# Optimization experiments

Measured on AMD Instinct MI355X. Metric: run time of the kernel, lower is better.

## Reference

```python
import jax, jax.numpy as jnp
import numpy as np

N, D, K = 16384, 256, 4096  # encoded vectors, embedding_dim, codebook_size


def setup_inputs() -> dict:
    key = jax.random.key(0)
    k_ze, k_cb = jax.random.split(key)
    ze = jax.random.normal(k_ze, (N, D), dtype=jnp.float32)
    codebook = jax.random.normal(k_cb, (K, D), dtype=jnp.float32)
    return {"ze": ze, "codebook": codebook}


def reference(ze, codebook):
    # Pairwise squared distances: ||ze||^2 + ||e||^2 - 2 ze e^T  -> [N, K]
    sq_norm = (
        jnp.sum(ze ** 2, axis=-1, keepdims=True)
        + jnp.sum(codebook ** 2, axis=1)
        - 2.0 * jnp.matmul(ze, codebook.T)
    )
    indices = jnp.argmin(sq_norm, axis=-1)            # [N]
    zq = jnp.take(codebook, indices, axis=0)          # [N, D] gather

    # VQ losses (stop-gradient mirrors .detach())
    vq_e_loss = jnp.mean((zq - jax.lax.stop_gradient(ze)) ** 2)
    vq_commit_loss = jnp.mean((jax.lax.stop_gradient(zq) - ze) ** 2)

    # perplexity: probs[i] = count_i / 10 (faithful to original, incl. /10)
    counts = jnp.zeros((K,), dtype=jnp.float32).at[indices].add(1.0)
    probs = counts / 10.0
    perplexity = jnp.exp(-jnp.sum(probs * jnp.log(probs + 1e-10)))

    return indices, zq, vq_e_loss, vq_commit_loss, perplexity
```

## Files before the change

### kernel.cpp

```cpp
#include <hip/hip_runtime.h>
#include <math.h>

#define N_TOT 16384
#define DIM   256
#define KCB   4096

typedef __attribute__((ext_vector_type(8)))  short s8v;
typedef __attribute__((ext_vector_type(16))) float f16v;

#define PK_OFF   32832
#define CBF_OFF  163904
#define WS_NEED  4358208ull
#define ZERO_W   36880

__device__ __forceinline__ void gload16(const void* g, void* l) {
  __builtin_amdgcn_global_load_lds(
      (const __attribute__((address_space(1))) unsigned int*)g,
      (__attribute__((address_space(3))) unsigned int*)l, 16, 0, 0);
}

__global__ __launch_bounds__(256)
void cb_prep_k(const float* __restrict__ cb, float* __restrict__ ws) {
  const int t = threadIdx.x, tile = blockIdx.x;
  for (int i = tile * 256 + t; i < ZERO_W; i += 128 * 256) ws[KCB + i] = 0.0f;

  const int col = t >> 3, j = t & 7;
  const int c0  = tile * 32;
  ushort* tb = (ushort*)((char*)ws + CBF_OFF) + (size_t)tile * 16384;
  const float* src = cb + (size_t)(c0 + col) * DIM;
  float s = 0.0f;
  #pragma unroll
  for (int ks = 0; ks < 16; ++ks) {
    #pragma unroll
    for (int kh = 0; kh < 2; ++kh) {
      float x = src[ks * 16 + kh * 8 + j];
      s += x * x;
      unsigned xb = __float_as_uint(x);
      unsigned hb = xb & 0xFFFF0000u;
      float lf = x - __uint_as_float(hb);
      tb[ks * 512 + kh * 256 + t]        = (ushort)(xb >> 16);
      tb[8192 + ks * 512 + kh * 256 + t] = (ushort)(__float_as_uint(lf) >> 16);
    }
  }
  s += __shfl_down(s, 4, 8);
  s += __shfl_down(s, 2, 8);
  s += __shfl_down(s, 1, 8);
  if (j == 0) ws[c0 + col] = s;
}

#define AP 260

__global__ __launch_bounds__(256, 2)
void vq_mfma_k(const float* __restrict__ ze, float* __restrict__ ws) {
  __shared__ __align__(16) char ldsU[65536];

  const int t    = threadIdx.x;
  const int lane = t & 63;
  const int w    = t >> 6;
  const int ln31 = lane & 31;
  const int hl   = lane >> 5;
  const int mb   = blockIdx.x >> 2;
  const int cq   = blockIdx.x & 3;
  const int m0   = mb * 128;

  const float* cbn = ws;
  unsigned long long* pk = (unsigned long long*)((char*)ws + PK_OFF);
  const char* cbF = (const char*)ws + CBF_OFF;

  s8v ah[16], al[16];
  float* Af = (float*)ldsU;
  for (int c = 0; c < 4; ++c) {
    __syncthreads();
    {
      int r  = t >> 3;
      int f0 = t & 7;
      const float* src = ze + (size_t)(m0 + c * 32 + r) * DIM;
      #pragma unroll
      for (int i = 0; i < 8; ++i) {
        int f = f0 + 8 * i;
        *(float4*)&Af[r * AP + f * 4] = *(const float4*)(src + f * 4);
      }
    }
    __syncthreads();
    if (w == c) {
      int rl = ln31;
      #pragma unroll
      for (int ks = 0; ks < 16; ++ks) {
        float4 x0 = *(const float4*)&Af[rl * AP + ks * 16 + hl * 8];
        float4 x1 = *(const float4*)&Af[rl * AP + ks * 16 + hl * 8 + 4];
        float xs[8] = {x0.x, x0.y, x0.z, x0.w, x1.x, x1.y, x1.z, x1.w};
        #pragma unroll
        for (int j = 0; j < 8; ++j) {
          unsigned xb = __float_as_uint(xs[j]);
          unsigned hb = xb & 0xFFFF0000u;
          float lf = xs[j] - __uint_as_float(hb);
          ah[ks][j] = (short)(xb >> 16);
          al[ks][j] = (short)(__float_as_uint(lf) >> 16);
        }
      }
    }
  }
  __syncthreads();

  char* bufs0 = ldsU;
  char* bufs1 = ldsU + 32768;
  const char* qbase = cbF + (size_t)cq * 32 * 32768;

  {
    const char* g = qbase + (size_t)w * 8192 + (size_t)lane * 16;
    char* lp = bufs0 + w * 8192;
    #pragma unroll
    for (int ii = 0; ii < 8; ++ii) gload16(g + ii * 1024, lp + ii * 1024);
  }

  float best[16];
  int   bidx[16];
  #pragma unroll
  for (int r = 0; r < 16; ++r) { best[r] = -1e30f; bidx[r] = 0; }

  #pragma unroll 1
  for (int tt = 0; tt < 32; ++tt) {
    __syncthreads();
    if (tt + 1 < 32) {
      const char* g = qbase + (size_t)(tt + 1) * 32768 + (size_t)w * 8192 + (size_t)lane * 16;
      char* lp = ((tt + 1) & 1 ? bufs1 : bufs0) + w * 8192;
      #pragma unroll
      for (int ii = 0; ii < 8; ++ii) gload16(g + ii * 1024, lp + ii * 1024);
    }

    const int   c0      = cq * 1024 + tt * 32;
    const float half_cv = 0.5f * cbn[c0 + ln31];
    const char* bc      = (tt & 1) ? bufs1 : bufs0;

    f16v hh, xx;
    #pragma unroll
    for (int r = 0; r < 16; ++r) { hh[r] = 0.0f; xx[r] = 0.0f; }

    #pragma unroll
    for (int ks = 0; ks < 16; ++ks) {
      s8v bh = *(const s8v*)(bc + ks * 1024 + lane * 16);
      s8v bl = *(const s8v*)(bc + 16384 + ks * 1024 + lane * 16);
      hh = __builtin_amdgcn_mfma_f32_32x32x16_bf16(ah[ks], bh, hh, 0, 0, 0);
      xx = __builtin_amdgcn_mfma_f32_32x32x16_bf16(ah[ks], bl, xx, 0, 0, 0);
      xx = __builtin_amdgcn_mfma_f32_32x32x16_bf16(al[ks], bh, xx, 0, 0, 0);
    }

    #pragma unroll
    for (int r = 0; r < 16; ++r) {
      float s = hh[r] + xx[r] - half_cv;
      if (s > best[r]) { best[r] = s; bidx[r] = c0 + ln31; }
    }
  }

  #pragma unroll
  for (int r = 0; r < 16; ++r) {
    float s = best[r];
    int   c = bidx[r];
    #pragma unroll
    for (int mk = 1; mk < 32; mk <<= 1) {
      float os = __shfl_xor(s, mk, 64);
      int   oc = __shfl_xor(c, mk, 64);
      if (os > s || (os == s && oc < c)) { s = os; c = oc; }
    }
    if (ln31 == 0) {
      int row = m0 + w * 32 + (r & 3) + 8 * (r >> 2) + 4 * hl;
      unsigned u = __float_as_uint(s);
      unsigned enc = (u & 0x80000000u) ? ~u : (u | 0x80000000u);
      unsigned long long p = ((unsigned long long)enc << 32) | (unsigned)(KCB - 1 - c);
      atomicMax(&pk[row], p);
    }
  }
}

__global__ __launch_bounds__(256)
void gather_k(const float* __restrict__ ze, const float* __restrict__ cb,
              float* __restrict__ ws, float* __restrict__ out) {
  __shared__ int sIdx[64];
  const int t  = threadIdx.x;
  const int m0 = blockIdx.x * 64;
  float* counts   = ws + KCB;
  float* loss_sum = ws + 2 * KCB;
  const unsigned long long* pk = (const unsigned long long*)((const char*)ws + PK_OFF);

  if (t < 64) {
    unsigned long long p = pk[m0 + t];
    int col = KCB - 1 - (int)(unsigned)(p & 0xFFFFFFFFull);
    out[m0 + t] = (float)col;
    sIdx[t] = col;
    atomicAdd(&counts[col], 1.0f);
  }
  __syncthreads();

  float* out_zq = out + N_TOT;
  const int w = t >> 6, ln = t & 63;
  float lsum = 0.0f;
  #pragma unroll
  for (int p = 0; p < 16; ++p) {
    int r = w + 4 * p;
    float4 cvv = *(const float4*)(cb + (size_t)sIdx[r] * DIM + ln * 4);
    float4 zv  = *(const float4*)(ze + (size_t)(m0 + r) * DIM + ln * 4);
    *(float4*)(out_zq + (size_t)(m0 + r) * DIM + ln * 4) = cvv;
    float dx = cvv.x - zv.x, dy = cvv.y - zv.y, dz = cvv.z - zv.z, dw = cvv.w - zv.w;
    lsum += dx * dx + dy * dy + dz * dz + dw * dw;
  }
  #pragma unroll
  for (int off = 32; off > 0; off >>= 1) lsum += __shfl_down(lsum, off, 64);
  if (ln == 0) atomicAdd(loss_sum, lsum);
}

__global__ void zero_ws_k(float* __restrict__ ws, int nw) {
  int i = blockIdx.x * 256 + threadIdx.x;
  if (i < nw) ws[KCB + i] = 0.0f;
}

__global__ void cbnorm_k(const float* __restrict__ cb, float* __restrict__ ws) {
  int row  = blockIdx.x * 4 + (threadIdx.x >> 6);
  int lane = threadIdx.x & 63;
  float4 v = *(const float4*)(cb + (size_t)row * DIM + lane * 4);
  float s = v.x*v.x + v.y*v.y + v.z*v.z + v.w*v.w;
  #pragma unroll
  for (int off = 32; off > 0; off >>= 1) s += __shfl_down(s, off, 64);
  if (lane == 0) ws[row] = s;
}

#define FBM 32
#define FBN 64
#define FBD 128
__global__ __launch_bounds__(256, 4)
void vq_main_k(const float* __restrict__ ze, const float* __restrict__ cb,
               float* __restrict__ ws, float* __restrict__ out) {
  __shared__ float As[FBM * FBD];
  __shared__ float Bs[FBN * FBD];
  __shared__ float red_d[FBM * 16];
  __shared__ int   red_i[FBM * 16];
  __shared__ int   sIdx[FBM];

  const int t  = threadIdx.x;
  const int tx = t & 15;
  const int ty = t >> 4;
  const int m0 = blockIdx.x * FBM;

  const float* cbn = ws;
  float* counts    = ws + KCB;
  float* loss_sum  = ws + 2 * KCB;

  float best0 = 1e30f, best1 = 1e30f;
  int   bidx0 = 0,     bidx1 = 0;
  const int sA = ty & 7;
  const int sB = tx & 7;

  for (int kt = 0; kt < KCB / FBN; ++kt) {
    float cbnj[4];
    #pragma unroll
    for (int j = 0; j < 4; ++j) cbnj[j] = cbn[kt * FBN + tx + 16 * j];
    float acc[2][4];
    #pragma unroll
    for (int i = 0; i < 2; ++i)
      #pragma unroll
      for (int j = 0; j < 4; ++j) acc[i][j] = 0.0f;

    for (int dc = 0; dc < DIM / FBD; ++dc) {
      __syncthreads();
      {
        int c  = t & 31;
        int rb = t >> 5;
        #pragma unroll
        for (int p = 0; p < 4; ++p) {
          int r = rb + 8 * p;
          float4 v = *(const float4*)(ze + (size_t)(m0 + r) * DIM + dc * FBD + c * 4);
          *(float4*)&As[r * FBD + ((c ^ (r & 7)) << 2)] = v;
        }
        #pragma unroll
        for (int p = 0; p < 8; ++p) {
          int r = rb + 8 * p;
          float4 v = *(const float4*)(cb + (size_t)(kt * FBN + r) * DIM + dc * FBD + c * 4);
          *(float4*)&Bs[r * FBD + ((c ^ (r & 7)) << 2)] = v;
        }
      }
      __syncthreads();
      #pragma unroll 8
      for (int ds = 0; ds < FBD / 4; ++ds) {
        float4 a0 = *(const float4*)&As[ty * FBD + ((ds ^ sA) << 2)];
        float4 a1 = *(const float4*)&As[(ty + 16) * FBD + ((ds ^ sA) << 2)];
        float4 b[4];
        #pragma unroll
        for (int j = 0; j < 4; ++j)
          b[j] = *(const float4*)&Bs[(tx + 16 * j) * FBD + ((ds ^ sB) << 2)];
        #pragma unroll
        for (int j = 0; j < 4; ++j) {
          acc[0][j] = fmaf(a0.x, b[j].x, acc[0][j]);
          acc[0][j] = fmaf(a0.y, b[j].y, acc[0][j]);
          acc[0][j] = fmaf(a0.z, b[j].z, acc[0][j]);
          acc[0][j] = fmaf(a0.w, b[j].w, acc[0][j]);
          acc[1][j] = fmaf(a1.x, b[j].x, acc[1][j]);
          acc[1][j] = fmaf(a1.y, b[j].y, acc[1][j]);
          acc[1][j] = fmaf(a1.z, b[j].z, acc[1][j]);
          acc[1][j] = fmaf(a1.w, b[j].w, acc[1][j]);
        }
      }
    }
    #pragma unroll
    for (int j = 0; j < 4; ++j) {
      int kg = kt * FBN + tx + 16 * j;
      float d0 = cbnj[j] - 2.0f * acc[0][j];
      float d1 = cbnj[j] - 2.0f * acc[1][j];
      if (d0 < best0) { best0 = d0; bidx0 = kg; }
      if (d1 < best1) { best1 = d1; bidx1 = kg; }
    }
  }

  __syncthreads();
  red_d[ty * 16 + tx] = best0;        red_i[ty * 16 + tx] = bidx0;
  red_d[(ty + 16) * 16 + tx] = best1; red_i[(ty + 16) * 16 + tx] = bidx1;
  __syncthreads();

  if (t < FBM) {
    float bd = red_d[t * 16]; int bi = red_i[t * 16];
    #pragma unroll
    for (int q = 1; q < 16; ++q) {
      float d = red_d[t * 16 + q]; int i2 = red_i[t * 16 + q];
      if (d < bd || (d == bd && i2 < bi)) { bd = d; bi = i2; }
    }
    out[m0 + t] = (float)bi;
    sIdx[t] = bi;
    atomicAdd(&counts[bi], 1.0f);
  }
  __syncthreads();

  float* out_zq = out + N_TOT;
  const int wv = t >> 6, ln = t & 63;
  float lsum = 0.0f;
  #pragma unroll
  for (int p = 0; p < 8; ++p) {
    int r = wv + 4 * p;
    float4 cvv = *(const float4*)(cb + (size_t)sIdx[r] * DIM + ln * 4);
    float4 zv  = *(const float4*)(ze + (size_t)(m0 + r) * DIM + ln * 4);
    *(float4*)(out_zq + (size_t)(m0 + r) * DIM + ln * 4) = cvv;
    float dx = cvv.x - zv.x, dy = cvv.y - zv.y, dz = cvv.z - zv.z, dw = cvv.w - zv.w;
    lsum += dx*dx + dy*dy + dz*dz + dw*dw;
  }
  #pragma unroll
  for (int off = 32; off > 0; off >>= 1) lsum += __shfl_down(lsum, off, 64);
  if (ln == 0) atomicAdd(loss_sum, lsum);
}

__global__ void finalize_k(const float* __restrict__ ws, float* __restrict__ out) {
  __shared__ float red[256];
  int t = threadIdx.x;
  const float* counts = ws + KCB;
  float s = 0.0f;
  for (int k = t; k < KCB; k += 256) {
    float p = counts[k] * 0.1f;
    s += p * logf(p + 1e-10f);
  }
  red[t] = s;
  __syncthreads();
  for (int q = 128; q > 0; q >>= 1) { if (t < q) red[t] += red[t + q]; __syncthreads(); }
  if (t == 0) {
    float loss = ws[2 * KCB] / (float)((size_t)N_TOT * DIM);
    float* o = out + N_TOT + (size_t)N_TOT * DIM;
    o[0] = loss;
    o[1] = loss;
    o[2] = expf(-red[0]);
  }
}

extern "C" void kernel_launch(void* const* d_in, const int* in_sizes, int n_in,
                              void* d_out, int out_size, void* d_ws, size_t ws_size,
                              hipStream_t stream) {
  const float* ze = (const float*)d_in[0];
  const float* cb = (const float*)d_in[1];
  float* out = (float*)d_out;
  float* ws  = (float*)d_ws;

  if (ws_size >= WS_NEED) {
    cb_prep_k<<<128, 256, 0, stream>>>(cb, ws);
    vq_mfma_k<<<512, 256, 0, stream>>>(ze, ws);
    gather_k<<<N_TOT / 64, 256, 0, stream>>>(ze, cb, ws, out);
  } else {
    zero_ws_k<<<(KCB + 1 + 255) / 256, 256, 0, stream>>>(ws, KCB + 1);
    cbnorm_k<<<KCB / 4, 256, 0, stream>>>(cb, ws);
    vq_main_k<<<N_TOT / FBM, 256, 0, stream>>>(ze, cb, ws, out);
  }
  finalize_k<<<1, 256, 0, stream>>>(ws, out);
}
```

Baseline: 200.6 us.

## Process 64 rows per wave to double codebook tile reuse in MFMA kernel

```diff
diff --git a/kernel.cpp b/kernel.cpp
--- a/kernel.cpp
+++ b/kernel.cpp
@@ -50,9 +50,9 @@
 
 #define AP 260
 
-__global__ __launch_bounds__(256, 2)
+__global__ __launch_bounds__(256, 1)
 void vq_mfma_k(const float* __restrict__ ze, float* __restrict__ ws) {
-  __shared__ __align__(16) char ldsU[65536];
+  __shared__ __align__(16) char ldsU[66560];
 
   const int t    = threadIdx.x;
   const int lane = t & 63;
@@ -61,41 +61,45 @@
   const int hl   = lane >> 5;
   const int mb   = blockIdx.x >> 2;
   const int cq   = blockIdx.x & 3;
-  const int m0   = mb * 128;
+  const int m0   = mb * 256;
 
   const float* cbn = ws;
   unsigned long long* pk = (unsigned long long*)((char*)ws + PK_OFF);
   const char* cbF = (const char*)ws + CBF_OFF;
 
-  s8v ah[16], al[16];
+  s8v ah[2][16], al[2][16];
   float* Af = (float*)ldsU;
+  #pragma unroll
   for (int c = 0; c < 4; ++c) {
     __syncthreads();
     {
-      int r  = t >> 3;
-      int f0 = t & 7;
-      const float* src = ze + (size_t)(m0 + c * 32 + r) * DIM;
+      int r  = t >> 2;
+      int f0 = t & 3;
+      const float* src = ze + (size_t)(m0 + c * 64 + r) * DIM;
       #pragma unroll
-      for (int i = 0; i < 8; ++i) {
-        int f = f0 + 8 * i;
+      for (int i = 0; i < 16; ++i) {
+        int f = f0 + 4 * i;
         *(float4*)&Af[r * AP + f * 4] = *(const float4*)(src + f * 4);
       }
     }
     __syncthreads();
     if (w == c) {
-      int rl = ln31;
       #pragma unroll
-      for (int ks = 0; ks < 16; ++ks) {
-        float4 x0 = *(const float4*)&Af[rl * AP + ks * 16 + hl * 8];
-        float4 x1 = *(const float4*)&Af[rl * AP + ks * 16 + hl * 8 + 4];
-        float xs[8] = {x0.x, x0.y, x0.z, x0.w, x1.x, x1.y, x1.z, x1.w};
-        #pragma unroll
-        for (int j = 0; j < 8; ++j) {
-          unsigned xb = __float_as_uint(xs[j]);
-          unsigned hb = xb & 0xFFFF0000u;
-          float lf = xs[j] - __uint_as_float(hb);
-          ah[ks][j] = (short)(xb >> 16);
-          al[ks][j] = (short)(__float_as_uint(lf) >> 16);
+      for (int rb = 0; rb < 2; ++rb) {
+        int rl = rb * 32 + ln31;
+        #pragma unroll
+        for (int ks = 0; ks < 16; ++ks) {
+          float4 x0 = *(const float4*)&Af[rl * AP + ks * 16 + hl * 8];
+          float4 x1 = *(const float4*)&Af[rl * AP + ks * 16 + hl * 8 + 4];
+          float xs[8] = {x0.x, x0.y, x0.z, x0.w, x1.x, x1.y, x1.z, x1.w};
+          #pragma unroll
+          for (int j = 0; j < 8; ++j) {
+            unsigned xb = __float_as_uint(xs[j]);
+            unsigned hb = xb & 0xFFFF0000u;
+            float lf = xs[j] - __uint_as_float(hb);
+            ah[rb][ks][j] = (short)(xb >> 16);
+            al[rb][ks][j] = (short)(__float_as_uint(lf) >> 16);
+          }
         }
       }
     }
@@ -113,10 +117,10 @@
     for (int ii = 0; ii < 8; ++ii) gload16(g + ii * 1024, lp + ii * 1024);
   }
 
-  float best[16];
-  int   bidx[16];
-  #pragma unroll
-  for (int r = 0; r < 16; ++r) { best[r] = -1e30f; bidx[r] = 0; }
+  float best[32];
+  int   bidx[32];
+  #pragma unroll
+  for (int r = 0; r < 32; ++r) { best[r] = -1e30f; bidx[r] = 0; }
 
   #pragma unroll 1
   for (int tt = 0; tt < 32; ++tt) {
@@ -132,28 +136,33 @@
     const float half_cv = 0.5f * cbn[c0 + ln31];
     const char* bc      = (tt & 1) ? bufs1 : bufs0;
 
-    f16v hh, xx;
-    #pragma unroll
-    for (int r = 0; r < 16; ++r) { hh[r] = 0.0f; xx[r] = 0.0f; }
+    f16v h0, x0, h1, x1;
+    #pragma unroll
+    for (int r = 0; r < 16; ++r) { h0[r] = 0.0f; x0[r] = 0.0f; h1[r] = 0.0f; x1[r] = 0.0f; }
 
     #pragma unroll
     for (int ks = 0; ks < 16; ++ks) {
       s8v bh = *(const s8v*)(bc + ks * 1024 + lane * 16);
       s8v bl = *(const s8v*)(bc + 16384 + ks * 1024 + lane * 16);
-      hh = __builtin_amdgcn_mfma_f32_32x32x16_bf16(ah[ks], bh, hh, 0, 0, 0);
-      xx = __builtin_amdgcn_mfma_f32_32x32x16_bf16(ah[ks], bl, xx, 0, 0, 0);
-      xx = __builtin_amdgcn_mfma_f32_32x32x16_bf16(al[ks], bh, xx, 0, 0, 0);
+      h0 = __builtin_amdgcn_mfma_f32_32x32x16_bf16(ah[0][ks], bh, h0, 0, 0, 0);
+      h1 = __builtin_amdgcn_mfma_f32_32x32x16_bf16(ah[1][ks], bh, h1, 0, 0, 0);
+      x0 = __builtin_amdgcn_mfma_f32_32x32x16_bf16(ah[0][ks], bl, x0, 0, 0, 0);
+      x1 = __builtin_amdgcn_mfma_f32_32x32x16_bf16(ah[1][ks], bl, x1, 0, 0, 0);
+      x0 = __builtin_amdgcn_mfma_f32_32x32x16_bf16(al[0][ks], bh, x0, 0, 0, 0);
+      x1 = __builtin_amdgcn_mfma_f32_32x32x16_bf16(al[1][ks], bh, x1, 0, 0, 0);
     }
 
     #pragma unroll
     for (int r = 0; r < 16; ++r) {
-      float s = hh[r] + xx[r] - half_cv;
-      if (s > best[r]) { best[r] = s; bidx[r] = c0 + ln31; }
-    }
-  }
-
-  #pragma unroll
-  for (int r = 0; r < 16; ++r) {
+      float s0 = h0[r] + x0[r] - half_cv;
+      if (s0 > best[r])      { best[r]      = s0; bidx[r]      = c0 + ln31; }
+      float s1 = h1[r] + x1[r] - half_cv;
+      if (s1 > best[16 + r]) { best[16 + r] = s1; bidx[16 + r] = c0 + ln31; }
+    }
+  }
+
+  #pragma unroll
+  for (int r = 0; r < 32; ++r) {
     float s = best[r];
     int   c = bidx[r];
     #pragma unroll
@@ -163,7 +172,8 @@
       if (os > s || (os == s && oc < c)) { s = os; c = oc; }
     }
     if (ln31 == 0) {
-      int row = m0 + w * 32 + (r & 3) + 8 * (r >> 2) + 4 * hl;
+      int rb = r >> 4, rr = r & 15;
+      int row = m0 + w * 64 + rb * 32 + (rr & 3) + 8 * (rr >> 2) + 4 * hl;
       unsigned u = __float_as_uint(s);
       unsigned enc = (u & 0x80000000u) ? ~u : (u | 0x80000000u);
       unsigned long long p = ((unsigned long long)enc << 32) | (unsigned)(KCB - 1 - c);
@@ -375,7 +385,7 @@
 
   if (ws_size >= WS_NEED) {
     cb_prep_k<<<128, 256, 0, stream>>>(cb, ws);
-    vq_mfma_k<<<512, 256, 0, stream>>>(ze, ws);
+    vq_mfma_k<<<256, 256, 0, stream>>>(ze, ws);
     gather_k<<<N_TOT / 64, 256, 0, stream>>>(ze, cb, ws, out);
   } else {
     zero_ws_k<<<(KCB + 1 + 255) / 256, 256, 0, stream>>>(ws, KCB + 1);
```

Result: slower. 217.2 us (+8.3%).
